# Performance work log

Measured on AMD Instinct MI355X. Metric: run time of the kernel, lower is better.

Reference implementation:

```python
import jax, jax.numpy as jnp
import numpy as np

E, L, M, F, S, P = 4, 10, 512, 128, 1000, 10  # envs, labels, max_sample, features, sample_size, batch_len


def setup_inputs() -> dict:
    key = jax.random.key(0)
    k1, k2, k3 = jax.random.split(key, 3)
    data_len = jax.random.randint(k1, (E, L), M // 2, M + 1, dtype=jnp.int32)
    matrix = jax.random.normal(k2, (E, L, M, F), dtype=jnp.float32)
    # zero out padded samples beyond data_len (as shape_to_matrix does)
    pad_mask = jnp.arange(M)[None, None, :, None] < data_len[:, :, None, None]
    matrix = matrix * pad_mask
    params = jnp.eye(F, dtype=jnp.float32) + 0.01 * jax.random.normal(k3, (F, F), dtype=jnp.float32)
    is_train_env = jnp.array([True, True, False, False])
    return {"matrix": matrix, "params": params, "data_len": data_len, "is_train_env": is_train_env}


def reference(matrix, params, data_len, is_train_env):
    lenf = data_len.astype(matrix.dtype)  # [E,L], torch keeps this as float32
    # __init__ preprocessing: normalize by mean std over sample dim (detached in torch)
    std = jax.lax.stop_gradient(jnp.std(matrix, axis=2).mean())
    mat = matrix / std
    # Silverman-style bandwidth on the normalized matrix (detached in torch)
    bw = jax.lax.stop_gradient(1.06 * (M ** (-1.0 / 5.0)) * jnp.std(mat, axis=2).mean())
    offset = jnp.exp(-0.5 / bw ** 2)
    proj = jnp.einsum('elmf,fg->elmg', mat, params)  # [E,L,M,F]
    left = jax.lax.stop_gradient(proj.min())   # .item() in torch -> constant
    right = jax.lax.stop_gradient(proj.max())
    delta = (right - left) / S
    x_grid = jnp.linspace(left, right, S)
    divisor = jnp.sqrt(2.0 * jnp.pi) * bw

    def step(acc, points):  # points: [P] grid chunk
        d2 = (proj[..., None] - points) ** 2                     # [E,L,M,F,P]
        s = jnp.sum(offset ** d2, axis=2)                        # [E,L,F,P]
        # remove contribution of zero-padded samples, then normalize by true count
        corr = (M - lenf)[:, :, None] * (offset ** (points ** 2))[None, None, :]  # [E,L,P]
        r = (s - corr[:, :, None, :]) / lenf[:, :, None, None]   # [E,L,F,P]
        d = jnp.sum(jnp.abs(r[:, None] - r[None, :]), axis=-1)   # [E,E,L,F] pairwise L1 over grid chunk
        return acc + d, None

    store_dis, _ = jax.lax.scan(step, jnp.zeros((E, E, L, F), proj.dtype), x_grid.reshape(S // P, P))
    store_dis = store_dis / divisor  # [E,E,L,F]

    idx = jnp.arange(E)
    upper = idx[:, None] < idx[None, :]                                   # all env pairs i<j
    train_pair = upper & is_train_env[:, None] & is_train_env[None, :]    # train env pairs i<j
    half = store_dis * (delta / 2.0)
    neg = jnp.array(-jnp.inf, half.dtype)
    test_results = jnp.where(upper[:, :, None, None], half, neg).max(axis=(0, 1))        # [L,F]
    train_results = jnp.where(train_pair[:, :, None, None], half, neg).max(axis=(0, 1))  # [L,F]
    train_dis = train_results.max(axis=0).mean()
    test_dis = test_results.max(axis=0).mean()
    return train_results, test_results, train_dis, test_dis
```

## Files before the change

kernel.cpp:

```cpp
#include <hip/hip_runtime.h>
#include <cmath>

#define E_ 4
#define L_ 10
#define M_ 512
#define F_ 128
#define S_ 1000

typedef unsigned int u32;
typedef _Float16 f16;
typedef __attribute__((ext_vector_type(8))) _Float16 v8h;
typedef __attribute__((ext_vector_type(4))) float v4f;

__device__ __forceinline__ float fexp2(float a){
#if __has_builtin(__builtin_amdgcn_exp2f)
  return __builtin_amdgcn_exp2f(a);
#else
  return exp2f(a);
#endif
}


__global__ __launch_bounds__(256) void k_pre(const float* __restrict__ mat,
                       const float* __restrict__ par,
                       float* __restrict__ projT, float* __restrict__ wsf){
  __shared__ float sm[512];
  int b = blockIdx.x, tid = threadIdx.x;
  if (b >= 1280){
    int el = b - 1280;
    int f = tid & 127, part = tid >> 7;
    const float* base = mat + ((size_t)el * M_ + part*256) * F_;
    float s = 0.f, s2 = 0.f;
    for (int i = 0; i < 256; i++){
      float v = base[i*F_ + f];
      s += v; s2 += v*v;
    }
    sm[tid] = s; sm[256 + tid] = s2;
    __syncthreads();
    if (tid < 128){
      wsf[2576 + el*128 + tid] = sm[tid] + sm[tid+128];
      wsf[7696 + el*128 + tid] = sm[256+tid] + sm[256+tid+128];
    }
    return;
  }
  int el = b >> 5, mt = (b & 31) * 16;
  int lane = tid & 63, wave = tid >> 6;
  int q = (lane >> 4) & 3, m16 = lane & 15;
  const float* arow = mat + ((size_t)el * M_ + mt + m16) * F_;
  v4f acc0 = {0.f,0.f,0.f,0.f}, acc1 = {0.f,0.f,0.f,0.f};
  #pragma unroll
  for (int c = 0; c < 4; c++){
    float4 a0 = *(const float4*)&arow[c*32 + q*8];
    float4 a1 = *(const float4*)&arow[c*32 + q*8 + 4];
    v8h af, b0, b1;
    af[0]=(f16)a0.x; af[1]=(f16)a0.y; af[2]=(f16)a0.z; af[3]=(f16)a0.w;
    af[4]=(f16)a1.x; af[5]=(f16)a1.y; af[6]=(f16)a1.z; af[7]=(f16)a1.w;
    const float* pb = par + (c*32 + q*8)*F_ + wave*32 + m16;
    #pragma unroll
    for (int j = 0; j < 8; j++){
      b0[j] = (f16)pb[j*F_];
      b1[j] = (f16)pb[j*F_ + 16];
    }
    acc0 = __builtin_amdgcn_mfma_f32_16x16x32_f16(af, b0, acc0, 0, 0, 0);
    acc1 = __builtin_amdgcn_mfma_f32_16x16x32_f16(af, b1, acc1, 0, 0, 0);
  }
  *(float4*)(projT + ((size_t)el*F_ + wave*32      + m16)*M_ + mt + q*4)
      = make_float4(acc0[0], acc0[1], acc0[2], acc0[3]);
  *(float4*)(projT + ((size_t)el*F_ + wave*32 + 16 + m16)*M_ + mt + q*4)
      = make_float4(acc1[0], acc1[1], acc1[2], acc1[3]);
  float lmin =  3.4e38f, lmax = -3.4e38f;
  #pragma unroll
  for (int r = 0; r < 4; r++){
    lmin = fminf(lmin, fminf(acc0[r], acc1[r]));
    lmax = fmaxf(lmax, fmaxf(acc0[r], acc1[r]));
  }
  #pragma unroll
  for (int d = 32; d >= 1; d >>= 1){
    lmin = fminf(lmin, __shfl_xor(lmin, d, 64));
    lmax = fmaxf(lmax, __shfl_xor(lmax, d, 64));
  }
  if (lane == 0){ sm[wave] = lmin; sm[8+wave] = lmax; }
  __syncthreads();
  if (tid == 0){
    wsf[16   + b] = fminf(fminf(sm[0], sm[1]), fminf(sm[2], sm[3]));
    wsf[1296 + b] = fmaxf(fmaxf(sm[8], sm[9]), fmaxf(sm[10], sm[11]));
  }
}

__global__ __launch_bounds__(1024) void k_red(float* __restrict__ wsf,
                                              float divisor, float k2c){
  __shared__ float rmn[1024], rmx[1024], rs[1024];
  int tid = threadIdx.x;
  float mn = 3.4e38f, mx = -3.4e38f, s = 0.f;
  for (int i = tid; i < 1280; i += 1024){
    mn = fminf(mn, wsf[16   + i]);
    mx = fmaxf(mx, wsf[1296 + i]);
  }
  for (int i = tid; i < 5120; i += 1024){
    float a  = wsf[2576 + i];
    float a2 = wsf[7696 + i];
    float mean = a * (1.0f/512.0f);
    float var  = a2 * (1.0f/512.0f) - mean*mean;
    s += sqrtf(fmaxf(var, 0.0f));
  }
  rmn[tid] = mn; rmx[tid] = mx; rs[tid] = s;
  __syncthreads();
  for (int g = 512; g >= 1; g >>= 1){
    if (tid < g){
      rmn[tid] = fminf(rmn[tid], rmn[tid+g]);
      rmx[tid] = fmaxf(rmx[tid], rmx[tid+g]);
      rs[tid] += rs[tid+g];
    }
    __syncthreads();
  }
  float rstd   = 5120.0f / rs[0];
  float leftS  = rmn[0] * rstd;
  float rightS = rmx[0] * rstd;
  float stepFS = (rightS - leftS) * (1.0f/999.0f);
  if (tid == 0){
    float inv2 = 1.0f / (2.0f * stepFS);
    wsf[0] = rstd * inv2;
    wsf[1] = leftS * inv2;
    wsf[2] = stepFS;
    wsf[3] = leftS;
    wsf[8] = ((rightS - leftS) * (1.0f/1000.0f)) * 0.5f / divisor;
  }
  float sh = 2.0f * stepFS;
  if (tid < 152){
    float v = 0.f;
    if (tid >= 8){
      int pr = (tid >> 1) - 4;
      int u  = pr - 34;
      float d = (tid & 1) ? (float)(2*u-1) * sh : (float)(2*u) * sh;
      v = (pr < 69) ? fexp2(k2c*d*d) : 0.f;
    }
    wsf[16 + tid] = v;
  }
  if (tid >= 256 && tid < 512){
    int idx = tid - 256;
    float xc = fmaf((float)(idx - 1), 4.0f*stepFS, leftS);
    wsf[168 + idx] = fexp2(k2c * xc * xc);
  }
}

__global__ __launch_bounds__(256) void k_kde(const float* __restrict__ projT,
                      const int* __restrict__ dlen, const float* __restrict__ wsf,
                      float* __restrict__ dpair){
  __shared__ __align__(16) float smem[5776];
  int b = blockIdx.x;
  int l = b >> 7, f = b & 127;
  int tid = threadIdx.x, wave = tid >> 6, lane = tid & 63;
  int e = wave;
  {
    int e0 = tid >> 7, mq = tid & 127;
    ((float4*)smem)[tid] =
      ((const float4*)(projT + (((size_t)e0 * L_ + l) * F_ + f) * M_))[mq];
    ((float4*)smem)[tid + 256] =
      ((const float4*)(projT + (((size_t)(e0+2) * L_ + l) * F_ + f) * M_))[mq];
  }
  float posScale = wsf[0], posOff = wsf[1];
  for (int idx = tid; idx < 824; idx += 256)
    ((float4*)(smem + 2048))[idx] = make_float4(0.f,0.f,0.f,0.f);
  if (tid < 38)
    ((float4*)(smem + 5344))[tid] = ((const float4*)(wsf + 16))[tid];
  if (tid >= 64 && tid < 128)
    ((float4*)(smem + 5496))[tid - 64] = ((const float4*)(wsf + 168))[tid - 64];
  __syncthreads();
  {
    float* hf = smem + 2048 + e*824;
    const float4* spw4 = (const float4*)(smem + e*512);
    float4 p0 = spw4[lane], p1 = spw4[lane + 64];
    float pv[8] = {p0.x,p0.y,p0.z,p0.w,p1.x,p1.y,p1.z,p1.w};
    #pragma unroll
    for (int i = 0; i < 8; i++){
      float pos = fmaf(pv[i], posScale, -posOff);
      float n = floorf(pos + 0.5f);
      float d = pos - n;
      float wm = 0.5f*(0.5f-d)*(0.5f-d);
      float wp = 0.5f*(0.5f+d)*(0.5f+d);
      float w0 = 0.75f - d*d;
      int b0 = (int)n + 71;
      int b1 = b0 + 1, b2 = b0 + 2;
      int W0 = b0 + ((b0>>3)<<1);
      int W1 = b1 + ((b1>>3)<<1);
      int W2 = b2 + ((b2>>3)<<1);
      atomicAdd(&hf[W0], wm);
      atomicAdd(&hf[W1], w0);
      atomicAdd(&hf[W2], wp);
    }
  }
  __syncthreads();
  float lenE = (float)dlen[e*L_ + l];
  float rlen = 1.0f / lenE;
  float padc = 512.0f - lenE;
  {
    const float2* sK2 = (const float2*)(smem + 5344);
    const float* hb = smem + 2048 + e*824;
    int wb = 8*lane;
    float2 c0 = sK2[72], c1 = sK2[73], c2 = sK2[74], c3 = sK2[75];
    float a0=0.f, a1=0.f, a2=0.f, a3=0.f;
    #pragma unroll 8
    for (int i = 1; i <= 72; i++){
      int w  = wb + 2*i;
      int wp_ = w + ((w>>3)<<1);
      float2 H = *(const float2*)&hb[wp_];
      a0 = fmaf(H.x, c0.x, fmaf(H.y, c0.y, a0));
      a1 = fmaf(H.x, c1.x, fmaf(H.y, c1.y, a1));
      a2 = fmaf(H.x, c2.x, fmaf(H.y, c2.y, a2));
      a3 = fmaf(H.x, c3.x, fmaf(H.y, c3.y, a3));
      c3 = c2; c2 = c1; c1 = c0; c0 = sK2[72 - i];
    }
    int o0 = 4*lane;
    float4 cr = *(const float4*)&smem[5496 + o0];
    float4 stv = make_float4((a0 - padc*cr.x)*rlen, (a1 - padc*cr.y)*rlen,
                             (a2 - padc*cr.z)*rlen, (a3 - padc*cr.w)*rlen);
    *(float4*)&smem[e*256 + o0] = stv;
  }
  __syncthreads();
  float ps[6] = {0,0,0,0,0,0};
  if (tid < 250){
    float x[4][4];
    #pragma unroll
    for (int ee=0; ee<4; ee++){
      const float* st = &smem[ee*256 + tid];
      x[ee][0]=st[0]; x[ee][1]=st[1]; x[ee][2]=st[2]; x[ee][3]=st[3];
    }
    #pragma unroll
    for (int k=0; k<4; k++){
      float u = (float)k * 0.25f;
      float um1 = u - 1.0f, um2 = u - 2.0f, up1 = u + 1.0f;
      float w0 = -u * um1 * um2 * (1.0f/6.0f);
      float w1 = up1 * um1 * um2 * 0.5f;
      float w2 = -u * up1 * um2 * 0.5f;
      float w3 = u * up1 * um1 * (1.0f/6.0f);
      float rr[4];
      #pragma unroll
      for (int ee=0; ee<4; ee++)
        rr[ee] = w0*x[ee][0] + w1*x[ee][1] + w2*x[ee][2] + w3*x[ee][3];
      ps[0] += fabsf(rr[0]-rr[1]);
      ps[1] += fabsf(rr[0]-rr[2]);
      ps[2] += fabsf(rr[0]-rr[3]);
      ps[3] += fabsf(rr[1]-rr[2]);
      ps[4] += fabsf(rr[1]-rr[3]);
      ps[5] += fabsf(rr[2]-rr[3]);
    }
  }
  #pragma unroll
  for (int pr=0; pr<6; pr++){
    float v = ps[pr];
    #pragma unroll
    for (int d=32; d>=1; d>>=1) v += __shfl_xor(v, d, 64);
    if (lane == 0) smem[5752 + wave*6 + pr] = v;
  }
  __syncthreads();
  if (tid < 6)
    dpair[tid*1280 + b] = smem[5752+tid] + smem[5758+tid] + smem[5764+tid] + smem[5770+tid];
}

__global__ void k_fin(const float* __restrict__ dpair, const float* __restrict__ wsf,
                      const int* __restrict__ istrain, float* __restrict__ out){
  __shared__ float str[1280], ste[1280];
  __shared__ float s1[128], s2[128];
  int tid = threadIdx.x;
  float hscale = wsf[8];
  bool t0 = istrain[0]!=0, t1 = istrain[1]!=0, t2 = istrain[2]!=0, t3 = istrain[3]!=0;
  bool trn[6] = { t0&&t1, t0&&t2, t0&&t3, t1&&t2, t1&&t3, t2&&t3 };
  for (int idx = tid; idx < 1280; idx += 256){
    float tmax = -INFINITY, trmax = -INFINITY;
    #pragma unroll
    for (int pr=0;pr<6;pr++){
      float h = dpair[pr*1280 + idx] * hscale;
      tmax = fmaxf(tmax, h);
      if (trn[pr]) trmax = fmaxf(trmax, h);
    }
    out[idx]        = trmax;
    out[1280 + idx] = tmax;
    str[idx] = trmax; ste[idx] = tmax;
  }
  __syncthreads();
  if (tid < 128){
    float m1 = -INFINITY, m2 = -INFINITY;
    for (int l=0;l<L_;l++){
      m1 = fmaxf(m1, str[l*F_ + tid]);
      m2 = fmaxf(m2, ste[l*F_ + tid]);
    }
    s1[tid] = m1; s2[tid] = m2;
  }
  __syncthreads();
  for (int g=64; g>=1; g>>=1){
    if (tid < g){ s1[tid] += s1[tid+g]; s2[tid] += s2[tid+g]; }
    __syncthreads();
  }
  if (tid == 0){
    out[2560] = s1[0] * (1.0f/128.0f);
    out[2561] = s2[0] * (1.0f/128.0f);
  }
}

extern "C" void kernel_launch(void* const* d_in, const int* in_sizes, int n_in,
                              void* d_out, int out_size, void* d_ws, size_t ws_size,
                              hipStream_t stream){
  const float* mat = (const float*)d_in[0];
  const float* par = (const float*)d_in[1];
  const int*  dlen = (const int*)d_in[2];
  const int*  istr = (const int*)d_in[3];
  float* out   = (float*)d_out;
  float* wsf   = (float*)d_ws;
  float* dpair = wsf + 12816;
  float* projT = wsf + 20496;

  double bw_d   = 1.06 * pow(512.0, -0.2);
  float  bw     = (float)bw_d;
  float  offset = expf(-0.5f / (bw*bw));
  float  k2c    = (float)(log((double)offset) * 1.4426950408889634);
  float  divisor = sqrtf(6.283185307179586f) * bw;

  k_pre <<<1320, 256, 0, stream>>>(mat, par, projT, wsf);
  k_red <<<1,   1024, 0, stream>>>(wsf, divisor, k2c);
  k_kde <<<1280, 256, 0, stream>>>(projT, dlen, wsf, dpair);
  k_fin <<<1,    256, 0, stream>>>(dpair, wsf, istr, out);
}
```

Baseline: 143.8 us.

## Vectorize stats reduction, load KDE projections into registers, simplify histogram indexing

Measured after the change: 142.2 us. About the same (-1.1%).

```diff
diff --git a/kernel.cpp b/kernel.cpp
--- a/kernel.cpp
+++ b/kernel.cpp
@@ -24,22 +24,37 @@
 __global__ __launch_bounds__(256) void k_pre(const float* __restrict__ mat,
                        const float* __restrict__ par,
                        float* __restrict__ projT, float* __restrict__ wsf){
-  __shared__ float sm[512];
+  __shared__ float sm[2048];
   int b = blockIdx.x, tid = threadIdx.x;
   if (b >= 1280){
     int el = b - 1280;
-    int f = tid & 127, part = tid >> 7;
-    const float* base = mat + ((size_t)el * M_ + part*256) * F_;
-    float s = 0.f, s2 = 0.f;
-    for (int i = 0; i < 256; i++){
-      float v = base[i*F_ + f];
-      s += v; s2 += v*v;
-    }
-    sm[tid] = s; sm[256 + tid] = s2;
+    int fq = (tid & 31) * 4, part = tid >> 5;
+    const float* base = mat + ((size_t)el * M_ + part*64) * F_;
+    float4 s  = make_float4(0.f,0.f,0.f,0.f);
+    float4 s2 = make_float4(0.f,0.f,0.f,0.f);
+    #pragma unroll 8
+    for (int i = 0; i < 64; i++){
+      float4 v = *(const float4*)&base[i*F_ + fq];
+      s.x += v.x; s.y += v.y; s.z += v.z; s.w += v.w;
+      s2.x += v.x*v.x; s2.y += v.y*v.y; s2.z += v.z*v.z; s2.w += v.w*v.w;
+    }
+    ((float4*)sm)[tid]       = s;
+    ((float4*)sm)[256 + tid] = s2;
     __syncthreads();
-    if (tid < 128){
-      wsf[2576 + el*128 + tid] = sm[tid] + sm[tid+128];
-      wsf[7696 + el*128 + tid] = sm[256+tid] + sm[256+tid+128];
+    for (int g = 4; g >= 1; g >>= 1){
+      if (part < g){
+        float4 o  = ((float4*)sm)[tid + g*32];
+        float4 o2 = ((float4*)sm)[256 + tid + g*32];
+        s.x += o.x; s.y += o.y; s.z += o.z; s.w += o.w;
+        s2.x += o2.x; s2.y += o2.y; s2.z += o2.z; s2.w += o2.w;
+        ((float4*)sm)[tid] = s;
+        ((float4*)sm)[256 + tid] = s2;
+      }
+      __syncthreads();
+    }
+    if (part == 0){
+      *(float4*)&wsf[2576 + el*128 + fq] = s;
+      *(float4*)&wsf[7696 + el*128 + fq] = s2;
     }
     return;
   }
@@ -146,31 +161,24 @@
 __global__ __launch_bounds__(256) void k_kde(const float* __restrict__ projT,
                       const int* __restrict__ dlen, const float* __restrict__ wsf,
                       float* __restrict__ dpair){
-  __shared__ __align__(16) float smem[5776];
+  __shared__ __align__(16) float smem[4752];
   int b = blockIdx.x;
   int l = b >> 7, f = b & 127;
   int tid = threadIdx.x, wave = tid >> 6, lane = tid & 63;
   int e = wave;
-  {
-    int e0 = tid >> 7, mq = tid & 127;
-    ((float4*)smem)[tid] =
-      ((const float4*)(projT + (((size_t)e0 * L_ + l) * F_ + f) * M_))[mq];
-    ((float4*)smem)[tid + 256] =
-      ((const float4*)(projT + (((size_t)(e0+2) * L_ + l) * F_ + f) * M_))[mq];
-  }
+  const float4* gp = (const float4*)(projT + (((size_t)e * L_ + l) * F_ + f) * M_);
+  float4 g0 = gp[lane], g1 = gp[lane + 64];
   float posScale = wsf[0], posOff = wsf[1];
   for (int idx = tid; idx < 824; idx += 256)
-    ((float4*)(smem + 2048))[idx] = make_float4(0.f,0.f,0.f,0.f);
+    ((float4*)(smem + 1024))[idx] = make_float4(0.f,0.f,0.f,0.f);
   if (tid < 38)
-    ((float4*)(smem + 5344))[tid] = ((const float4*)(wsf + 16))[tid];
+    ((float4*)(smem + 4320))[tid] = ((const float4*)(wsf + 16))[tid];
   if (tid >= 64 && tid < 128)
-    ((float4*)(smem + 5496))[tid - 64] = ((const float4*)(wsf + 168))[tid - 64];
+    ((float4*)(smem + 4472))[tid - 64] = ((const float4*)(wsf + 168))[tid - 64];
   __syncthreads();
   {
-    float* hf = smem + 2048 + e*824;
-    const float4* spw4 = (const float4*)(smem + e*512);
-    float4 p0 = spw4[lane], p1 = spw4[lane + 64];
-    float pv[8] = {p0.x,p0.y,p0.z,p0.w,p1.x,p1.y,p1.z,p1.w};
+    float* hf = smem + 1024 + e*824;
+    float pv[8] = {g0.x,g0.y,g0.z,g0.w,g1.x,g1.y,g1.z,g1.w};
     #pragma unroll
     for (int i = 0; i < 8; i++){
       float pos = fmaf(pv[i], posScale, -posOff);
@@ -194,16 +202,13 @@
   float rlen = 1.0f / lenE;
   float padc = 512.0f - lenE;
   {
-    const float2* sK2 = (const float2*)(smem + 5344);
-    const float* hb = smem + 2048 + e*824;
-    int wb = 8*lane;
+    const float2* sK2 = (const float2*)(smem + 4320);
+    const float* hl = smem + 1024 + e*824 + 10*lane;
     float2 c0 = sK2[72], c1 = sK2[73], c2 = sK2[74], c3 = sK2[75];
     float a0=0.f, a1=0.f, a2=0.f, a3=0.f;
-    #pragma unroll 8
+    #pragma unroll
     for (int i = 1; i <= 72; i++){
-      int w  = wb + 2*i;
-      int wp_ = w + ((w>>3)<<1);
-      float2 H = *(const float2*)&hb[wp_];
+      float2 H = *(const float2*)&hl[2*i + 2*(i>>2)];
       a0 = fmaf(H.x, c0.x, fmaf(H.y, c0.y, a0));
       a1 = fmaf(H.x, c1.x, fmaf(H.y, c1.y, a1));
       a2 = fmaf(H.x, c2.x, fmaf(H.y, c2.y, a2));
@@ -211,7 +216,7 @@
       c3 = c2; c2 = c1; c1 = c0; c0 = sK2[72 - i];
     }
     int o0 = 4*lane;
-    float4 cr = *(const float4*)&smem[5496 + o0];
+    float4 cr = *(const float4*)&smem[4472 + o0];
     float4 stv = make_float4((a0 - padc*cr.x)*rlen, (a1 - padc*cr.y)*rlen,
                              (a2 - padc*cr.z)*rlen, (a3 - padc*cr.w)*rlen);
     *(float4*)&smem[e*256 + o0] = stv;
@@ -250,11 +255,11 @@
     float v = ps[pr];
     #pragma unroll
     for (int d=32; d>=1; d>>=1) v += __shfl_xor(v, d, 64);
-    if (lane == 0) smem[5752 + wave*6 + pr] = v;
+    if (lane == 0) smem[4728 + wave*6 + pr] = v;
   }
   __syncthreads();
   if (tid < 6)
-    dpair[tid*1280 + b] = smem[5752+tid] + smem[5758+tid] + smem[5764+tid] + smem[5770+tid];
+    dpair[tid*1280 + b] = smem[4728+tid] + smem[4734+tid] + smem[4740+tid] + smem[4746+tid];
 }
 
 __global__ void k_fin(const float* __restrict__ dpair, const float* __restrict__ wsf,
```
